# Optimization experiments

Measured on AMD Instinct MI355X. Metric: run time of the kernel, lower is better.

## Reference

```python
import jax, jax.numpy as jnp
import numpy as np

B, S, HID = 1, 2048, 2048
H, KH, D = 16, 8, 128          # query heads, kv heads, head_dim
GROUPS = H // KH                # num_key_value_groups = 2
EPS = 1e-6
SCALE = D ** -0.5
NEG = -1e9


def rmsnorm(x, w):
    # torch.nn.RMSNorm over last dim with learned weight
    return x * jax.lax.rsqrt(jnp.mean(x * x, axis=-1, keepdims=True) + EPS) * w


def rope(x, cos, sin):
    # x: [b, s, h, d]; cos/sin: [s, d//2]  (rotate-half style, matching apply_rotary_emb_single)
    half = x.shape[-1] // 2
    xr, xi = x[..., :half], x[..., half:]
    c = cos[None, :, None, :]
    s = sin[None, :, None, :]
    return jnp.concatenate([xr * c - xi * s, xr * s + xi * c], axis=-1)


def setup_inputs() -> dict:
    key = jax.random.key(0)
    ks = jax.random.split(key, 8)
    hidden_states = jax.random.normal(ks[0], (B, S, HID), jnp.float32)
    # real RoPE angle tables (theta=1e6, Qwen3-style), shape [S, D//2]
    inv_freq = 1.0 / (1e6 ** (np.arange(0, D, 2, dtype=np.float32) / D))
    ang = np.arange(S, dtype=np.float32)[:, None] * inv_freq[None, :]
    freqs_cos = jnp.asarray(np.cos(ang), jnp.float32)
    freqs_sin = jnp.asarray(np.sin(ang), jnp.float32)
    # additive causal mask [1, S, S]
    causal = jnp.tril(jnp.ones((S, S), jnp.bool_))
    atten_mask = jnp.where(causal, 0.0, NEG).astype(jnp.float32)[None]
    # learned params (no bias: attention_bias=False)
    Wq = jax.random.normal(ks[1], (H * D, HID), jnp.float32) * 0.02
    Wk = jax.random.normal(ks[2], (KH * D, HID), jnp.float32) * 0.02
    Wv = jax.random.normal(ks[3], (KH * D, HID), jnp.float32) * 0.02
    Wo = jax.random.normal(ks[4], (HID, H * D), jnp.float32) * 0.02
    q_norm_w = 1.0 + 0.01 * jax.random.normal(ks[5], (D,), jnp.float32)
    k_norm_w = 1.0 + 0.01 * jax.random.normal(ks[6], (D,), jnp.float32)
    return {"hidden_states": hidden_states, "freqs_cos": freqs_cos, "freqs_sin": freqs_sin,
            "atten_mask": atten_mask, "Wq": Wq, "Wk": Wk, "Wv": Wv, "Wo": Wo,
            "q_norm_w": q_norm_w, "k_norm_w": k_norm_w}


def reference(hidden_states, freqs_cos, freqs_sin, atten_mask, Wq, Wk, Wv, Wo, q_norm_w, k_norm_w):
    b, s, _ = hidden_states.shape
    q = (hidden_states @ Wq.T).reshape(b, s, H, D)
    k = (hidden_states @ Wk.T).reshape(b, s, KH, D)
    v = (hidden_states @ Wv.T).reshape(b, s, KH, D)
    q = rope(rmsnorm(q, q_norm_w), freqs_cos, freqs_sin)
    k = rope(rmsnorm(k, k_norm_w), freqs_cos, freqs_sin)
    # GQA: head i uses kv head i // GROUPS -> repeat kv heads in-order
    k_exp = jnp.repeat(k, GROUPS, axis=2)  # [b, s, H, d]
    v_exp = jnp.repeat(v, GROUPS, axis=2)
    scores = jnp.einsum('bshd,bthd->bhst', q, k_exp) * SCALE + atten_mask[:, None, :, :]
    attn = jax.nn.softmax(scores, axis=-1)
    y = jnp.einsum('bhst,bthd->bshd', attn, v_exp).reshape(b, s, H * D)
    y = y @ Wo.T
    # output_new_cache_only: last-position k (post-norm/RoPE) and raw v per kv head
    k_new = jnp.transpose(k[:, -1], (1, 0, 2))  # [KH, b, D]
    v_new = jnp.transpose(v[:, -1], (1, 0, 2))  # [KH, b, D]
    return y, k_new, v_new
```

## Files before the change

### kernel.cpp

```cpp
#include <hip/hip_runtime.h>
#include <hip/hip_bf16.h>
#include <math.h>

#define S_LEN 2048
#define HID 2048
#define NH 16
#define NKH 8
#define HD 128
#define QKV_N 4096
#define SCALE 0.08838834764831845f
#define EPS 1e-6f
#define LOG2E 1.4426950408889634f
#define QSCALE (SCALE * LOG2E)

typedef __hip_bfloat16 bf16;
typedef unsigned int u32;
typedef __bf16 bf16x8 __attribute__((ext_vector_type(8)));
typedef float f32x4 __attribute__((ext_vector_type(4)));

#define MFMA(a, b, c) __builtin_amdgcn_mfma_f32_16x16x32_bf16(a, b, c, 0, 0, 0)

static __device__ __forceinline__ bf16x8 ld_frag(const bf16* p) {
    return __builtin_bit_cast(bf16x8, *(const uint4*)p);
}

static __device__ __forceinline__ void gload_lds16(const void* g, void* l) {
    __builtin_amdgcn_global_load_lds(
        (const __attribute__((address_space(1))) u32*)g,
        (__attribute__((address_space(3))) u32*)l, 16, 0, 0);
}

__global__ __launch_bounds__(256) void cvt5(
    const float* __restrict__ s0, const float* __restrict__ s1,
    const float* __restrict__ s2, const float* __restrict__ s3,
    const float* __restrict__ s4,
    bf16* __restrict__ d0, bf16* __restrict__ d1, bf16* __restrict__ d2,
    bf16* __restrict__ d3, bf16* __restrict__ d4)
{
    int i = blockIdx.x * 256 + threadIdx.x;
    const float* s; bf16* d; int off;
    if (i < (1 << 20))                   { s = s0; d = d0; off = 0; }
    else if (i < (2 << 20))              { s = s1; d = d1; off = 1 << 20; }
    else if (i < (2 << 20) + (1 << 19))  { s = s2; d = d2; off = 2 << 20; }
    else if (i < (3 << 20))              { s = s3; d = d3; off = (2 << 20) + (1 << 19); }
    else                                 { s = s4; d = d4; off = 3 << 20; }
    int j = i - off;
    float4 v = ((const float4*)s)[j];
    bf16* p = d + 4 * (size_t)j;
    p[0] = __float2bfloat16(v.x);
    p[1] = __float2bfloat16(v.y);
    p[2] = __float2bfloat16(v.z);
    p[3] = __float2bfloat16(v.w);
}

__global__ __launch_bounds__(256, 2) void gemm_qkv(
    const bf16* __restrict__ A, const bf16* __restrict__ B,
    bf16* __restrict__ qkvb, bf16* __restrict__ vT,
    const float* __restrict__ fcos, const float* __restrict__ fsin,
    const float* __restrict__ qw, const float* __restrict__ kw,
    float* __restrict__ knew, float* __restrict__ vnew)
{
    __shared__ bf16 As[2][128 * 64];
    __shared__ bf16 Bs[2][128 * 64];
    __shared__ float red[2][2][64];
    const int tid = threadIdx.x;
    const int n0 = blockIdx.x * 128, m0 = blockIdx.y * 128;
    const int w = tid >> 6, lane = tid & 63;
    const int l15 = lane & 15, quad = lane >> 4;
    const int wr = (w >> 1) * 64;
    const int wcg = (w & 1) * 32;

    f32x4 acc[4][4];
    #pragma unroll
    for (int i = 0; i < 4; ++i)
        #pragma unroll
        for (int j = 0; j < 4; ++j)
            acc[i][j] = f32x4{0.f, 0.f, 0.f, 0.f};

    const int srow8 = lane >> 3;
    const int sls = ((lane & 7) ^ srow8) * 8;

    auto stage = [&](int k0, int nb) {
        #pragma unroll
        for (int j = 0; j < 8; ++j) {
            int c = 8 * w + j;
            if (c < 16) {
                int row = c * 8 + srow8;
                gload_lds16(A + (size_t)(m0 + row) * HID + k0 + sls, &As[nb][c * 512]);
            } else {
                int row = (c - 16) * 8 + srow8;
                gload_lds16(B + (size_t)(n0 + row) * HID + k0 + sls, &Bs[nb][(c - 16) * 512]);
            }
        }
    };

    stage(0, 0);
    for (int kt = 0; kt < HID / 64; ++kt) {
        const int pp = kt & 1;
        __syncthreads();
        if (kt + 1 < HID / 64) stage((kt + 1) * 64, pp ^ 1);

        #pragma unroll
        for (int kc = 0; kc < 2; ++kc) {
            const int ph = ((kc * 4 + quad) ^ (l15 & 7)) * 8;
            bf16x8 av[4], bv[4];
            #pragma unroll
            for (int i = 0; i < 4; ++i)
                av[i] = ld_frag(&As[pp][(wr + i * 16 + l15) * 64 + ph]);
            #pragma unroll
            for (int j = 0; j < 4; ++j)
                bv[j] = ld_frag(&Bs[pp][(wcg + (j & 1) * 16 + (j >> 1) * 64 + l15) * 64 + ph]);
            #pragma unroll
            for (int i = 0; i < 4; ++i)
                #pragma unroll
                for (int j = 0; j < 4; ++j)
                    acc[i][j] = MFMA(av[i], bv[j], acc[i][j]);
        }
    }

    const int hblk = n0 >> 7;
    if (hblk < 24) {
        float ssq[4][4];
        #pragma unroll
        for (int i = 0; i < 4; ++i)
            #pragma unroll
            for (int rr = 0; rr < 4; ++rr) {
                float ss = 0.f;
                #pragma unroll
                for (int j = 0; j < 4; ++j) ss += acc[i][j][rr] * acc[i][j][rr];
                ss += __shfl_xor(ss, 1);
                ss += __shfl_xor(ss, 2);
                ss += __shfl_xor(ss, 4);
                ss += __shfl_xor(ss, 8);
                ssq[i][rr] = ss;
                if (l15 == 0)
                    red[w >> 1][w & 1][i * 16 + quad * 4 + rr] = ss;
            }
        __syncthreads();

        const float* wgt = (hblk < 16) ? qw : kw;
        float wv[4];
        #pragma unroll
        for (int j = 0; j < 4; ++j)
            wv[j] = wgt[wcg + (j & 1) * 16 + (j >> 1) * 64 + l15];
        const size_t cb = (hblk < 16) ? (size_t)hblk * HD
                                      : (size_t)HID + (size_t)(hblk - 16) * HD;

        #pragma unroll
        for (int i = 0; i < 4; ++i)
            #pragma unroll
            for (int rr = 0; rr < 4; ++rr) {
                int rloc = i * 16 + quad * 4 + rr;
                int srow = m0 + wr + rloc;
                float tot = ssq[i][rr] + red[w >> 1][(w & 1) ^ 1][rloc];
                float rrn = rsqrtf(tot * (1.0f / 128.0f) + EPS);
                float x[4], res[4];
                #pragma unroll
                for (int j = 0; j < 4; ++j) x[j] = acc[i][j][rr] * rrn * wv[j];
                #pragma unroll
                for (int j2 = 0; j2 < 2; ++j2) {
                    float c = fcos[srow * 64 + wcg + j2 * 16 + l15];
                    float s = fsin[srow * 64 + wcg + j2 * 16 + l15];
                    res[j2]     = x[j2] * c - x[j2 + 2] * s;
                    res[j2 + 2] = x[j2] * s + x[j2 + 2] * c;
                }
                if (hblk < 16) {
                    #pragma unroll
                    for (int j = 0; j < 4; ++j)
                        qkvb[(size_t)srow * QKV_N + cb + wcg + (j & 1) * 16 +
                             (j >> 1) * 64 + l15] = __float2bfloat16(res[j] * QSCALE);
                } else {
                    #pragma unroll
                    for (int j = 0; j < 4; ++j)
                        qkvb[(size_t)srow * QKV_N + cb + wcg + (j & 1) * 16 +
                             (j >> 1) * 64 + l15] = __float2bfloat16(res[j]);
                    if (srow == S_LEN - 1) {
                        #pragma unroll
                        for (int j = 0; j < 4; ++j)
                            knew[(hblk - 16) * HD + wcg + (j & 1) * 16 +
                                 (j >> 1) * 64 + l15] = res[j];
                    }
                }
            }
    } else {
        const int kh = hblk - 24;
        #pragma unroll
        for (int i = 0; i < 4; ++i) {
            int rowbase = m0 + wr + i * 16 + quad * 4;
            #pragma unroll
            for (int j = 0; j < 4; ++j) {
                int d = wcg + (j & 1) * 16 + (j >> 1) * 64 + l15;
                union { uint2 u; bf16 hh[4]; } pk;
                #pragma unroll
                for (int r = 0; r < 4; ++r)
                    pk.hh[r] = __float2bfloat16(acc[i][j][r]);
                *(uint2*)&vT[(size_t)(kh * HD + d) * S_LEN + rowbase] = pk.u;
                if (rowbase == S_LEN - 4)
                    vnew[kh * HD + d] = acc[i][j][3];
            }
        }
    }
}

__global__ __launch_bounds__(256, 2) void gemm_n64(
    const bf16* __restrict__ A, const bf16* __restrict__ B,
    float* __restrict__ C, int M, int N, int K)
{
    __shared__ bf16 As[2][128 * 64];
    __shared__ bf16 Bs[2][64 * 64];
    const int tid = threadIdx.x;
    const int n0 = blockIdx.x * 64, m0 = blockIdx.y * 128;
    const int w = tid >> 6, lane = tid & 63;
    const int l15 = lane & 15, quad = lane >> 4;

    f32x4 acc[2][4];
    #pragma unroll
    for (int i = 0; i < 2; ++i)
        #pragma unroll
        for (int j = 0; j < 4; ++j)
            acc[i][j] = f32x4{0.f, 0.f, 0.f, 0.f};

    const int srow8 = lane >> 3;
    const int sls = ((lane & 7) ^ srow8) * 8;

    auto stage = [&](int k0, int nb) {
        #pragma unroll
        for (int j = 0; j < 6; ++j) {
            int c = 6 * w + j;
            if (c < 16) {
                int row = c * 8 + srow8;
                gload_lds16(A + (size_t)(m0 + row) * K + k0 + sls, &As[nb][c * 512]);
            } else {
                int row = (c - 16) * 8 + srow8;
                gload_lds16(B + (size_t)(n0 + row) * K + k0 + sls, &Bs[nb][(c - 16) * 512]);
            }
        }
    };

    stage(0, 0);
    for (int kt = 0; kt < K / 64; ++kt) {
        const int pp = kt & 1;
        __syncthreads();
        if (kt + 1 < K / 64) stage((kt + 1) * 64, pp ^ 1);

        #pragma unroll
        for (int kc = 0; kc < 2; ++kc) {
            const int ph = ((kc * 4 + quad) ^ (l15 & 7)) * 8;
            bf16x8 av[2], bv[4];
            av[0] = ld_frag(&As[pp][(w * 32 + l15) * 64 + ph]);
            av[1] = ld_frag(&As[pp][(w * 32 + 16 + l15) * 64 + ph]);
            #pragma unroll
            for (int j = 0; j < 4; ++j)
                bv[j] = ld_frag(&Bs[pp][(j * 16 + l15) * 64 + ph]);
            #pragma unroll
            for (int i = 0; i < 2; ++i)
                #pragma unroll
                for (int j = 0; j < 4; ++j)
                    acc[i][j] = MFMA(av[i], bv[j], acc[i][j]);
        }
    }

    #pragma unroll
    for (int i = 0; i < 2; ++i)
        #pragma unroll
        for (int j = 0; j < 4; ++j)
            #pragma unroll
            for (int r = 0; r < 4; ++r)
                C[(size_t)(m0 + w * 32 + i * 16 + quad * 4 + r) * N +
                  n0 + j * 16 + l15] = acc[i][j][r];
}

__global__ __launch_bounds__(256, 2) void attn_mfma(
    const bf16* __restrict__ qkvb, const bf16* __restrict__ vT,
    bf16* __restrict__ outb)
{
    __shared__ bf16 Ks[2][64 * 128];
    __shared__ bf16 Vs[2][128 * 64];
    __shared__ bf16 Ps[4][16 * 72];

    const int x = blockIdx.x;
    const int h = blockIdx.y, kvh = h >> 1;
    int a = (x & 1) ? (31 - (x >> 1)) : (x >> 1);
    const int qb = (h < 8) ? a : 31 - a;
    const int tid = threadIdx.x, w = tid >> 6, lane = tid & 63;
    const int l15 = lane & 15, quad = lane >> 4;
    const int qw0 = qb * 64 + w * 16;

    bf16x8 qf[4];
    #pragma unroll
    for (int dk = 0; dk < 4; ++dk)
        qf[dk] = ld_frag(qkvb + (size_t)(qw0 + l15) * QKV_N +
                         h * HD + dk * 32 + quad * 8);

    f32x4 o[8];
    #pragma unroll
    for (int dt = 0; dt < 8; ++dt) o[dt] = f32x4{0.f, 0.f, 0.f, 0.f};
    float l_st = 0.f;

    auto stage = [&](int t, int nb) {
        const int kt0 = t * 64;
        if (w < 2) {
            #pragma unroll
            for (int c = 0; c < 8; ++c) {
                int chunk = w * 8 + c;
                int row = 4 * chunk + (lane >> 4);
                int ls = (lane & 15) ^ (row & 15);
                gload_lds16(qkvb + (size_t)(kt0 + row) * QKV_N + HID +
                            kvh * HD + ls * 8,
                            &Ks[nb][chunk * 512]);
            }
        } else {
            #pragma unroll
            for (int c = 0; c < 8; ++c) {
                int chunk = (w - 2) * 8 + c;
                int row = 8 * chunk + (lane >> 3);
                int ls = (lane & 7) ^ ((lane >> 3) & 7);
                gload_lds16(vT + (size_t)(kvh * HD + row) * S_LEN + kt0 + ls * 8,
                            &Vs[nb][chunk * 512]);
            }
        }
    };

    stage(0, 0);
    for (int t = 0; t <= qb; ++t) {
        const int pp = t & 1;
        const int kt0 = t * 64;
        __syncthreads();
        if (t < qb) stage(t + 1, pp ^ 1);

        f32x4 sc[4];
        #pragma unroll
        for (int mt = 0; mt < 4; ++mt) sc[mt] = f32x4{0.f, 0.f, 0.f, 0.f};
        #pragma unroll
        for (int dk = 0; dk < 4; ++dk)
            #pragma unroll
            for (int mt = 0; mt < 4; ++mt) {
                bf16x8 kf = ld_frag(&Ks[pp][(mt * 16 + l15) * 128 +
                                            (((dk * 4 + quad) ^ l15) & 15) * 8]);
                sc[mt] = MFMA(kf, qf[dk], sc[mt]);
            }

        if (kt0 + 63 > qw0) {
            #pragma unroll
            for (int mt = 0; mt < 4; ++mt)
                #pragma unroll
                for (int r = 0; r < 4; ++r) {
                    int kg = kt0 + mt * 16 + quad * 4 + r;
                    if (kg > qw0 + l15) sc[mt][r] = -1e30f;
                }
        }

        #pragma unroll
        for (int mt = 0; mt < 4; ++mt) {
            union { uint2 u; bf16 hh[4]; } pk;
            #pragma unroll
            for (int r = 0; r < 4; ++r) {
                float p = exp2f(sc[mt][r]);
                pk.hh[r] = __float2bfloat16(p);
                l_st += p;
            }
            *(uint2*)&Ps[w][l15 * 72 + mt * 16 + quad * 4] = pk.u;
        }

        #pragma unroll
        for (int kc = 0; kc < 2; ++kc) {
            bf16x8 pf = ld_frag(&Ps[w][l15 * 72 + kc * 32 + quad * 8]);
            #pragma unroll
            for (int dt = 0; dt < 8; ++dt) {
                bf16x8 vf = ld_frag(&Vs[pp][(dt * 16 + l15) * 64 +
                                            (((kc * 4 + quad) ^ (l15 & 7)) * 8)]);
                o[dt] = MFMA(vf, pf, o[dt]);
            }
        }
    }

    l_st += __shfl_xor(l_st, 16, 64);
    l_st += __shfl_xor(l_st, 32, 64);
    float inv = 1.0f / l_st;
    int qg = qw0 + l15;
    #pragma unroll
    for (int dt = 0; dt < 8; ++dt) {
        union { uint2 u; bf16 hh[4]; } pk;
        #pragma unroll
        for (int r = 0; r < 4; ++r)
            pk.hh[r] = __float2bfloat16(o[dt][r] * inv);
        *(uint2*)&outb[(size_t)qg * HID + h * HD + dt * 16 + quad * 4] = pk.u;
    }
}

extern "C" void kernel_launch(void* const* d_in, const int* in_sizes, int n_in,
                              void* d_out, int out_size, void* d_ws, size_t ws_size,
                              hipStream_t stream) {
    const float* hidden = (const float*)d_in[0];
    const float* fcos   = (const float*)d_in[1];
    const float* fsin   = (const float*)d_in[2];
    const float* Wq = (const float*)d_in[4];
    const float* Wk = (const float*)d_in[5];
    const float* Wv = (const float*)d_in[6];
    const float* Wo = (const float*)d_in[7];
    const float* qw = (const float*)d_in[8];
    const float* kw = (const float*)d_in[9];
    float* out = (float*)d_out;

    bf16* qkvb  = (bf16*)d_ws;
    bf16* vT    = qkvb + (size_t)S_LEN * QKV_N;
    bf16* attnb = vT + (size_t)NKH * HD * S_LEN;
    bf16* wqkvb = attnb + (size_t)S_LEN * HID;
    bf16* hidb  = wqkvb + (size_t)QKV_N * HID;
    bf16* wob   = hidb + (size_t)S_LEN * HID;

    float* knew = out + (size_t)S_LEN * HID;
    float* vnew = knew + NKH * HD;

    cvt5<<<16384, 256, 0, stream>>>(
        hidden, Wq, Wk, Wv, Wo,
        hidb, wqkvb, wqkvb + (size_t)HID * HID,
        wqkvb + (size_t)(HID + NKH * HD) * HID, wob);

    gemm_qkv<<<dim3(QKV_N / 128, S_LEN / 128), 256, 0, stream>>>(
        hidb, wqkvb, qkvb, vT, fcos, fsin, qw, kw, knew, vnew);

    attn_mfma<<<dim3(32, NH), 256, 0, stream>>>(qkvb, vT, attnb);

    gemm_n64<<<dim3(HID / 64, S_LEN / 128), 256, 0, stream>>>(
        attnb, wob, out, S_LEN, HID, HID);
}
```

Before: 240.8 us.

## Enlarge QKV GEMM tile to 256x128 with 512 threads and triple-buffered pipeline

The QKV projection GEMM now uses 512-thread blocks computing 256x128 output tiles. Its LDS buffers go from double to triple buffering, with loads issued two k-steps ahead and split across the two k-chunks. The loop uses explicit s_waitcnt/s_barrier sequencing, sched_barrier and setprio around the MFMA bursts to overlap global loads with compute. This aims to improve data reuse and hide memory latency. The cost is more LDS per block (about 144KB, which likely limits occupancy to one block per CU) and fragile hand-written synchronization. The epilogue (norm/rope) must handle the larger M tile correctly, and the unchanged wr/red indexing in that unseen code is a correctness risk.

```diff
diff --git a/kernel.cpp b/kernel.cpp
--- a/kernel.cpp
+++ b/kernel.cpp
@@ -53,18 +53,18 @@
     p[3] = __float2bfloat16(v.w);
 }
 
-__global__ __launch_bounds__(256, 2) void gemm_qkv(
+__global__ __launch_bounds__(512, 2) void gemm_qkv(
     const bf16* __restrict__ A, const bf16* __restrict__ B,
     bf16* __restrict__ qkvb, bf16* __restrict__ vT,
     const float* __restrict__ fcos, const float* __restrict__ fsin,
     const float* __restrict__ qw, const float* __restrict__ kw,
     float* __restrict__ knew, float* __restrict__ vnew)
 {
-    __shared__ bf16 As[2][128 * 64];
-    __shared__ bf16 Bs[2][128 * 64];
-    __shared__ float red[2][2][64];
+    __shared__ bf16 As[3][256 * 64];
+    __shared__ bf16 Bs[3][128 * 64];
+    __shared__ float red[4][2][64];
     const int tid = threadIdx.x;
-    const int n0 = blockIdx.x * 128, m0 = blockIdx.y * 128;
+    const int n0 = blockIdx.x * 128, m0 = blockIdx.y * 256;
     const int w = tid >> 6, lane = tid & 63;
     const int l15 = lane & 15, quad = lane >> 4;
     const int wr = (w >> 1) * 64;
@@ -80,25 +80,31 @@
     const int srow8 = lane >> 3;
     const int sls = ((lane & 7) ^ srow8) * 8;
 
-    auto stage = [&](int k0, int nb) {
-        #pragma unroll
-        for (int j = 0; j < 8; ++j) {
-            int c = 8 * w + j;
-            if (c < 16) {
+    auto stage3 = [&](int k0, int nb, int half) {
+        #pragma unroll
+        for (int j = 0; j < 3; ++j) {
+            int c = 6 * w + half * 3 + j;
+            if (c < 32) {
                 int row = c * 8 + srow8;
                 gload_lds16(A + (size_t)(m0 + row) * HID + k0 + sls, &As[nb][c * 512]);
             } else {
-                int row = (c - 16) * 8 + srow8;
-                gload_lds16(B + (size_t)(n0 + row) * HID + k0 + sls, &Bs[nb][(c - 16) * 512]);
+                int row = (c - 32) * 8 + srow8;
+                gload_lds16(B + (size_t)(n0 + row) * HID + k0 + sls, &Bs[nb][(c - 32) * 512]);
             }
         }
     };
 
-    stage(0, 0);
-    for (int kt = 0; kt < HID / 64; ++kt) {
-        const int pp = kt & 1;
-        __syncthreads();
-        if (kt + 1 < HID / 64) stage((kt + 1) * 64, pp ^ 1);
+    stage3(0, 0, 0);  stage3(0, 0, 1);
+    stage3(64, 1, 0); stage3(64, 1, 1);
+    asm volatile("s_waitcnt vmcnt(6)" ::: "memory");
+    asm volatile("s_barrier" ::: "memory");
+
+    int bt = 0;
+    #pragma unroll 1
+    for (int t = 0; t < 32; ++t) {
+        const bool ds = (t < 30);
+        const int nbs = (bt == 0) ? 2 : bt - 1;
+        const int k0s = (t + 2) * 64;
 
         #pragma unroll
         for (int kc = 0; kc < 2; ++kc) {
@@ -106,16 +112,29 @@
             bf16x8 av[4], bv[4];
             #pragma unroll
             for (int i = 0; i < 4; ++i)
-                av[i] = ld_frag(&As[pp][(wr + i * 16 + l15) * 64 + ph]);
+                av[i] = ld_frag(&As[bt][(wr + i * 16 + l15) * 64 + ph]);
             #pragma unroll
             for (int j = 0; j < 4; ++j)
-                bv[j] = ld_frag(&Bs[pp][(wcg + (j & 1) * 16 + (j >> 1) * 64 + l15) * 64 + ph]);
+                bv[j] = ld_frag(&Bs[bt][(wcg + (j & 1) * 16 + (j >> 1) * 64 + l15) * 64 + ph]);
+            if (ds) stage3(k0s, nbs, kc);
+            asm volatile("s_barrier" ::: "memory");
+            asm volatile("s_waitcnt lgkmcnt(0)" ::: "memory");
+            __builtin_amdgcn_sched_barrier(0);
+            __builtin_amdgcn_s_setprio(1);
             #pragma unroll
             for (int i = 0; i < 4; ++i)
                 #pragma unroll
                 for (int j = 0; j < 4; ++j)
                     acc[i][j] = MFMA(av[i], bv[j], acc[i][j]);
-        }
+            __builtin_amdgcn_s_setprio(0);
+            __builtin_amdgcn_sched_barrier(0);
+            if (kc == 1) {
+                if (t < 30)       asm volatile("s_waitcnt vmcnt(6)" ::: "memory");
+                else if (t == 30) asm volatile("s_waitcnt vmcnt(0)" ::: "memory");
+            }
+            asm volatile("s_barrier" ::: "memory");
+        }
+        bt = (bt == 2) ? 0 : bt + 1;
     }
 
     const int hblk = n0 >> 7;
@@ -417,7 +436,7 @@
         hidb, wqkvb, wqkvb + (size_t)HID * HID,
         wqkvb + (size_t)(HID + NKH * HD) * HID, wob);
 
-    gemm_qkv<<<dim3(QKV_N / 128, S_LEN / 128), 256, 0, stream>>>(
+    gemm_qkv<<<dim3(QKV_N / 128, S_LEN / 256), 512, 0, stream>>>(
         hidb, wqkvb, qkvb, vT, fcos, fsin, qw, kw, knew, vnew);
 
     attn_mfma<<<dim3(32, NH), 256, 0, stream>>>(qkvb, vT, attnb);
```

Result: no change. 244.2 us (+1.4%).
